# Optimization experiments

Hardware: AMD Instinct MI355X
Metric: run time of the kernel (lower is better)

Reference implementation:

```python
import jax, jax.numpy as jnp
import numpy as np

D_MODEL = 1024
D_FF = 4096
N_EXPERTS = 8
D_EXPERT = D_FF // N_EXPERTS  # 512
TOP_K = 2
LB_WEIGHT = 0.01
B, S = 4, 2048


def setup_inputs() -> dict:
    key = jax.random.key(0)
    ks = jax.random.split(key, 8)
    x = jax.random.normal(ks[0], (B, S, D_MODEL), dtype=jnp.float32)
    # per-expert FFN params stacked on expert axis
    w1 = jax.random.normal(ks[1], (N_EXPERTS, D_MODEL, D_EXPERT), dtype=jnp.float32) * (1.0 / np.sqrt(D_MODEL))
    b1 = jnp.zeros((N_EXPERTS, D_EXPERT), dtype=jnp.float32)
    w2 = jax.random.normal(ks[2], (N_EXPERTS, D_EXPERT, D_MODEL), dtype=jnp.float32) * (1.0 / np.sqrt(D_EXPERT))
    b2 = jnp.zeros((N_EXPERTS, D_MODEL), dtype=jnp.float32)
    centroids = jax.random.normal(ks[3], (N_EXPERTS, D_MODEL), dtype=jnp.float32) * 0.02
    w_route = jax.random.normal(ks[4], (N_EXPERTS, D_MODEL), dtype=jnp.float32) * (1.0 / np.sqrt(D_MODEL))
    return {"x": x, "w1": w1, "b1": b1, "w2": w2, "b2": b2,
            "centroids": centroids, "w_route": w_route}


def _top_k_softmax(logits, k):
    # softmax restricted to the top-k logits per token; zeros elsewhere
    vals, _ = jax.lax.top_k(logits, k)          # (..., k)
    thresh = vals[..., -1:]                     # kth-largest value
    masked = jnp.where(logits >= thresh, logits, -jnp.inf)
    return jax.nn.softmax(masked, axis=-1)


def reference(x, w1, b1, w2, b2, centroids, w_route):
    eps = 1e-12
    x_norm = x / jnp.maximum(jnp.linalg.norm(x, axis=-1, keepdims=True), eps)
    c_norm = centroids / jnp.maximum(jnp.linalg.norm(centroids, axis=-1, keepdims=True), eps)
    cos_scores = jnp.einsum('bsd,ed->bse', x_norm, c_norm)
    route_scores = jnp.einsum('bsd,ed->bse', x, w_route)
    logits = cos_scores + route_scores                       # (B,S,E)
    gates = _top_k_softmax(logits, TOP_K)                    # (B,S,E)
    # all experts computed on all tokens (dense MoE, masked combine)
    h = jax.nn.gelu(jnp.einsum('bsd,edh->bseh', x, w1) + b1, approximate=False)
    expert_out = jnp.einsum('bseh,ehd->bsed', h, w2) + b2    # (B,S,E,D)
    out = jnp.einsum('bse,bsed->bsd', gates, expert_out)
    return out
```

## Files before the change

kernel.cpp:

```cpp
#include <hip/hip_runtime.h>
#include <hip/hip_bf16.h>
#include <math.h>

#define T_TOK 8192
#define DM 1024
#define DE 512
#define NE 8
#define DFF 4096

#define CO_X   0
#define CO_W1  8388608
#define CO_W2  12582912
#define CO_B1  16777216
#define CO_B2  16781312
#define CO_CE  16789504
#define CO_WR  16797696
#define CO_TOT 16805888

#define WS_GATE2 256
#define WS_B32   65792
#define WS_TOP2  262400
#define WS_TOK   295168
#define WS_AE    360704
#define WS_AG    426240
#define WS_INV   491776
#define WS_CONV  557312
#define WS_HC    34169088
#define WS_OC    50946304

typedef __attribute__((ext_vector_type(8))) __bf16 bf16x8;
typedef __attribute__((ext_vector_type(4))) __bf16 bf16x4;
typedef __attribute__((ext_vector_type(4))) float f32x4;

__device__ __forceinline__ f32x4 ld4(const void* p, size_t off, int md)
{
  f32x4 r;
  if (md){
    bf16x4 v = *(const bf16x4*)((const __bf16*)p + off);
    #pragma unroll
    for (int j = 0; j < 4; j++) r[j] = (float)v[j];
  } else {
    r = *(const f32x4*)((const float*)p + off);
  }
  return r;
}

__device__ __forceinline__ void async_ld16(const __bf16* g, __bf16* l)
{
  __builtin_amdgcn_global_load_lds(
      (const __attribute__((address_space(1))) unsigned int*)g,
      (__attribute__((address_space(3))) unsigned int*)l, 16, 0, 0);
}

__global__ __launch_bounds__(256) void detect_k(const void* xp, const void* cp,
                                                int* meta, int* b32)
{
  const int tid = threadIdx.x;
  const float* xf = (const float*)xp;
  int ok = 0;
  for (int i = tid; i < 1024; i += 256){
    float a = fabsf(xf[i]);
    if (a > 1e-8f && a < 100.f) ok++;
  }
  __shared__ int cnt;
  __shared__ int flg;
  if (tid == 0) cnt = 0;
  __syncthreads();
  atomicAdd(&cnt, ok);
  __syncthreads();
  if (tid == 0){ flg = (cnt > 512) ? 0 : 1; meta[0] = flg; }
  __syncthreads();
  const int md = flg;

  const int e = tid >> 5, i = tid & 31;
  float ss = 0.f;
  for (int j = 0; j < 32; j++){
    size_t d = (size_t)e * DM + i + j * 32;
    float v = md ? (float)((const __bf16*)cp)[d] : ((const float*)cp)[d];
    ss += v * v;
  }
  #pragma unroll
  for (int m = 1; m < 32; m <<= 1) ss += __shfl_xor(ss, m, 64);
  float* cinv = (float*)(meta + 48);
  if (i == 0) cinv[e] = 1.f / fmaxf(sqrtf(ss), 1e-12f);

  b32[tid] = 0;
  if (tid < 8) meta[16 + tid] = 0;
}

__global__ __launch_bounds__(256) void convert_k(
    const float* __restrict__ x, const float* __restrict__ b1,
    const float* __restrict__ b2, const float* __restrict__ ce,
    const float* __restrict__ wr, __bf16* __restrict__ dst,
    const int* __restrict__ meta)
{
  if (meta[0]) return;
  const size_t i = ((size_t)blockIdx.x * 256 + threadIdx.x) * 4;
  const float* src; size_t doff;
  if (i < 8388608){ src = x + i; doff = CO_X + i; }
  else {
    size_t j = i - 8388608;
    doff = CO_B1 + j;
    if      (j < 4096)  src = b1 + j;
    else if (j < 12288) src = b2 + (j - 4096);
    else if (j < 20480) src = ce + (j - 12288);
    else                src = wr + (j - 20480);
  }
  f32x4 v = *(const f32x4*)src;
  bf16x4 o;
  #pragma unroll
  for (int j = 0; j < 4; j++) o[j] = (__bf16)v[j];
  *(bf16x4*)(dst + doff) = o;
}

__global__ __launch_bounds__(256) void transp_k(
    const void* w1q, const void* w2q, __bf16* __restrict__ conv,
    const int* __restrict__ meta)
{
  const int md = meta[0];
  __shared__ __bf16 tile[32][33];
  const int b = blockIdx.x, tid = threadIdx.x;
  const int ty = tid >> 5, tx = tid & 31;

  const void* src; __bf16* dst; int ldS, ldD, i0, j0; size_t soff, doffb;
  if (b < 4096){
    const int e = b >> 9, t = b & 511;
    i0 = (t >> 4) << 5; j0 = (t & 15) << 5;
    ldS = DE; ldD = DM;
    soff = (size_t)e * DM * DE;
    dst = conv + CO_W1; doffb = (size_t)e * DE * DM;
    src = md ? (const void*)((const __bf16*)w1q) : (const void*)((const float*)w1q);
  } else {
    const int e = (b - 4096) >> 9, t = (b - 4096) & 511;
    i0 = (t >> 5) << 5; j0 = (t & 31) << 5;
    ldS = DM; ldD = DE;
    soff = (size_t)e * DE * DM;
    dst = conv + CO_W2; doffb = (size_t)e * DM * DE;
    src = md ? (const void*)((const __bf16*)w2q) : (const void*)((const float*)w2q);
  }

  #pragma unroll
  for (int rr = 0; rr < 4; rr++){
    const int r = rr * 8 + ty;
    const size_t s = soff + (size_t)(i0 + r) * ldS + j0 + tx;
    tile[r][tx] = md ? ((const __bf16*)src)[s] : (__bf16)((const float*)src)[s];
  }
  __syncthreads();
  #pragma unroll
  for (int rr = 0; rr < 4; rr++){
    const int r = rr * 8 + ty;
    dst[doffb + (size_t)(j0 + r) * ldD + i0 + tx] = tile[tx][r];
  }
}

__global__ __launch_bounds__(256) void route_k(
    const void* __restrict__ xp, const void* __restrict__ cp,
    const void* __restrict__ wp, const int* __restrict__ meta,
    float2* __restrict__ gate2, int* __restrict__ top2, int* __restrict__ b32)
{
  const int md = meta[0];
  const float* cinv = (const float*)(meta + 48);
  const int tid = threadIdx.x;
  const int g = tid >> 4, l = tid & 15;
  const int t = blockIdx.x * 16 + g;

  __shared__ int hist[8];
  if (tid < 8) hist[tid] = 0;
  __syncthreads();

  float xx = 0.f, cd[NE], wd[NE];
  #pragma unroll
  for (int e = 0; e < NE; e++){ cd[e] = 0.f; wd[e] = 0.f; }

  const size_t xbase = (size_t)t * DM;
  for (int j = 0; j < 16; j++){
    const int d0 = j * 64 + l * 4;
    f32x4 xv = ld4(xp, xbase + d0, md);
    xx += xv[0]*xv[0] + xv[1]*xv[1] + xv[2]*xv[2] + xv[3]*xv[3];
    #pragma unroll
    for (int e = 0; e < NE; e++){
      f32x4 cv = ld4(cp, (size_t)e * DM + d0, md);
      f32x4 wv = ld4(wp, (size_t)e * DM + d0, md);
      cd[e] += xv[0]*cv[0] + xv[1]*cv[1] + xv[2]*cv[2] + xv[3]*cv[3];
      wd[e] += xv[0]*wv[0] + xv[1]*wv[1] + xv[2]*wv[2] + xv[3]*wv[3];
    }
  }
  #pragma unroll
  for (int m = 1; m < 16; m <<= 1){
    xx += __shfl_xor(xx, m, 64);
    #pragma unroll
    for (int e = 0; e < NE; e++){
      cd[e] += __shfl_xor(cd[e], m, 64);
      wd[e] += __shfl_xor(wd[e], m, 64);
    }
  }

  if (l == 0){
    const float rxn = 1.f / fmaxf(sqrtf(xx), 1e-12f);
    float logits[NE];
    #pragma unroll
    for (int e = 0; e < NE; e++) logits[e] = cd[e] * rxn * cinv[e] + wd[e];
    float m1 = -1e30f; int i1 = 0;
    #pragma unroll
    for (int e = 0; e < NE; e++) if (logits[e] > m1){ m1 = logits[e]; i1 = e; }
    float m2 = -1e30f; int i2 = (i1 == 0) ? 1 : 0;
    #pragma unroll
    for (int e = 0; e < NE; e++)
      if (e != i1 && logits[e] > m2){ m2 = logits[e]; i2 = e; }
    float denom = 0.f, ex1 = 0.f, ex2 = 0.f;
    #pragma unroll
    for (int e = 0; e < NE; e++){
      if (logits[e] >= m2){
        float ee = expf(logits[e] - m1);
        denom += ee;
        if (e == i1) ex1 = ee;
        if (e == i2) ex2 = ee;
      }
    }
    const float inv = 1.f / denom;
    gate2[t] = make_float2(ex1 * inv, ex2 * inv);
    top2[t] = i1 | (i2 << 8);
    atomicAdd(&hist[i1], 1);
    atomicAdd(&hist[i2], 1);
  }
  __syncthreads();
  if (tid < 8) atomicAdd(&b32[(blockIdx.x >> 4) * 8 + tid], hist[tid]);
}

__global__ void offsets_k(int* meta, int* b32)
{
  const int l = threadIdx.x;
  int running = 0;
  for (int e = 0; e < NE; e++){
    int v = (l < 32) ? b32[l * 8 + e] : 0;
    int incl = v;
    #pragma unroll
    for (int ofs = 1; ofs < 32; ofs <<= 1){
      int n = __shfl_up(incl, ofs, 64);
      if (l >= ofs) incl += n;
    }
    int tot = __shfl(incl, 31, 64);
    if (l < 32) b32[l * 8 + e] = running + (incl - v);
    if (l == 0){ meta[16 + e] = tot; meta[32 + e] = running; }
    running += tot;
  }
}

__global__ __launch_bounds__(256) void place_k(
    const int* __restrict__ top2, const float2* __restrict__ gate2,
    const int* __restrict__ b32, int* __restrict__ tok, int* __restrict__ ae,
    float* __restrict__ agv, int* __restrict__ inv)
{
  __shared__ int cur[8];
  if (threadIdx.x < 8) cur[threadIdx.x] = b32[blockIdx.x * 8 + threadIdx.x];
  __syncthreads();
  const int t = blockIdx.x * 256 + threadIdx.x;
  const int p = top2[t];
  const float2 gg = gate2[t];
  const int e1 = p & 255, e2 = (p >> 8) & 255;
  const int s1 = atomicAdd(&cur[e1], 1);
  tok[s1] = t; ae[s1] = e1; agv[s1] = gg.x; inv[2 * t] = s1;
  const int s2 = atomicAdd(&cur[e2], 1);
  tok[s2] = t; ae[s2] = e2; agv[s2] = gg.y; inv[2 * t + 1] = s2;
}

__device__ __forceinline__ bool find_tile(const int* meta, int tm,
                                          int& e, int& base, int& valid)
{
  for (e = 0; e < NE; e++){
    const int cnt = meta[16 + e];
    const int nt = (cnt + 127) >> 7;
    if (tm < nt){
      const int r0 = tm << 7;
      base = meta[32 + e] + r0;
      valid = cnt - r0;
      return true;
    }
    tm -= nt;
  }
  return false;
}

__global__ __launch_bounds__(256) void gemm1g_k(
    const void* xq, const void* b1q, const __bf16* __restrict__ conv,
    const int* __restrict__ meta, const int* __restrict__ tok,
    const float* __restrict__ agv, __bf16* __restrict__ Hc)
{
  const int md = meta[0];
  const __bf16* X  = md ? (const __bf16*)xq : conv + CO_X;
  const __bf16* WT = conv + CO_W1;
  const __bf16* bb = md ? (const __bf16*)b1q : conv + CO_B1;

  int e, base, valid;
  if (!find_tile(meta, blockIdx.x, e, base, valid)) return;
  const int n0 = blockIdx.y * 128;

  __shared__ __attribute__((aligned(16))) __bf16 As[128 * 32];
  __shared__ __attribute__((aligned(16))) __bf16 Bs[128 * 32];

  const int tid = threadIdx.x;
  const int wv = tid >> 6, lane = tid & 63;
  const int q = lane >> 4, ln = lane & 15;
  const int wm = (wv >> 1) * 64, wn = (wv & 1) * 64;
  f32x4 acc[4][4] = {};

  const int sr = tid >> 2, sc = (tid & 3) * 8;
  const int t0 = tok[base + ((sr      < valid) ? sr      : 0)];
  const int t1 = tok[base + ((sr + 64 < valid) ? sr + 64 : 0)];
  const __bf16* Ag0 = X + (size_t)t0 * DM + sc;
  const __bf16* Ag1 = X + (size_t)t1 * DM + sc;
  const __bf16* Bg0 = WT + (size_t)e * (DE * DM) + (size_t)(n0 + sr) * DM + sc;
  const __bf16* Bg1 = Bg0 + (size_t)64 * DM;

  for (int k0 = 0; k0 < DM; k0 += 32){
    __syncthreads();
    async_ld16(Ag0 + k0, As + tid * 8);
    async_ld16(Ag1 + k0, As + 2048 + tid * 8);
    async_ld16(Bg0 + k0, Bs + tid * 8);
    async_ld16(Bg1 + k0, Bs + 2048 + tid * 8);
    __syncthreads();

    bf16x8 af[4], bf[4];
    #pragma unroll
    for (int mi = 0; mi < 4; mi++)
      af[mi] = *(const bf16x8*)&As[(wm + mi * 16 + ln) * 32 + q * 8];
    #pragma unroll
    for (int ni = 0; ni < 4; ni++)
      bf[ni] = *(const bf16x8*)&Bs[(wn + ni * 16 + ln) * 32 + q * 8];
    #pragma unroll
    for (int mi = 0; mi < 4; mi++)
      #pragma unroll
      for (int ni = 0; ni < 4; ni++)
        acc[mi][ni] = __builtin_amdgcn_mfma_f32_16x16x32_bf16(
            af[mi], bf[ni], acc[mi][ni], 0, 0, 0);
  }

  const int coln = n0 + wn;
  float bset[4];
  #pragma unroll
  for (int ni = 0; ni < 4; ni++)
    bset[ni] = (float)bb[e * DE + coln + ni * 16 + ln];
  #pragma unroll
  for (int mi = 0; mi < 4; mi++){
    #pragma unroll
    for (int r = 0; r < 4; r++){
      const int row = wm + mi * 16 + q * 4 + r;
      if (row < valid){
        const int slot = base + row;
        const float g = agv[slot];
        #pragma unroll
        for (int ni = 0; ni < 4; ni++){
          float v = acc[mi][ni][r] + bset[ni];
          float h = 0.5f * v * (1.0f + erff(v * 0.70710678118654752f));
          Hc[(size_t)slot * DE + coln + ni * 16 + ln] = (__bf16)(g * h);
        }
      }
    }
  }
}

__global__ __launch_bounds__(256) void gemm2g_k(
    const __bf16* __restrict__ Hc, const __bf16* __restrict__ conv,
    const int* __restrict__ meta, __bf16* __restrict__ Oc)
{
  const __bf16* WT = conv + CO_W2;

  int e, base, valid;
  if (!find_tile(meta, blockIdx.x, e, base, valid)) return;
  const int n0 = blockIdx.y * 128;

  __shared__ __attribute__((aligned(16))) __bf16 As[128 * 32];
  __shared__ __attribute__((aligned(16))) __bf16 Bs[128 * 32];

  const int tid = threadIdx.x;
  const int wv = tid >> 6, lane = tid & 63;
  const int q = lane >> 4, ln = lane & 15;
  const int wm = (wv >> 1) * 64, wn = (wv & 1) * 64;
  f32x4 acc[4][4] = {};

  const int sr = tid >> 2, sc = (tid & 3) * 8;
  const int r0 = (sr      < valid) ? sr      : 0;
  const int r1 = (sr + 64 < valid) ? sr + 64 : 0;
  const __bf16* Ag0 = Hc + (size_t)(base + r0) * DE + sc;
  const __bf16* Ag1 = Hc + (size_t)(base + r1) * DE + sc;
  const __bf16* Bg0 = WT + (size_t)e * (DM * DE) + (size_t)(n0 + sr) * DE + sc;
  const __bf16* Bg1 = Bg0 + (size_t)64 * DE;

  for (int k0 = 0; k0 < DE; k0 += 32){
    __syncthreads();
    async_ld16(Ag0 + k0, As + tid * 8);
    async_ld16(Ag1 + k0, As + 2048 + tid * 8);
    async_ld16(Bg0 + k0, Bs + tid * 8);
    async_ld16(Bg1 + k0, Bs + 2048 + tid * 8);
    __syncthreads();

    bf16x8 af[4], bf[4];
    #pragma unroll
    for (int mi = 0; mi < 4; mi++)
      af[mi] = *(const bf16x8*)&As[(wm + mi * 16 + ln) * 32 + q * 8];
    #pragma unroll
    for (int ni = 0; ni < 4; ni++)
      bf[ni] = *(const bf16x8*)&Bs[(wn + ni * 16 + ln) * 32 + q * 8];
    #pragma unroll
    for (int mi = 0; mi < 4; mi++)
      #pragma unroll
      for (int ni = 0; ni < 4; ni++)
        acc[mi][ni] = __builtin_amdgcn_mfma_f32_16x16x32_bf16(
            af[mi], bf[ni], acc[mi][ni], 0, 0, 0);
  }

  #pragma unroll
  for (int mi = 0; mi < 4; mi++){
    #pragma unroll
    for (int r = 0; r < 4; r++){
      const int row = wm + mi * 16 + q * 4 + r;
      if (row < valid){
        const int slot = base + row;
        #pragma unroll
        for (int ni = 0; ni < 4; ni++)
          Oc[(size_t)slot * DM + n0 + wn + ni * 16 + ln] = (__bf16)acc[mi][ni][r];
      }
    }
  }
}

__global__ __launch_bounds__(256) void combine_k(
    const __bf16* __restrict__ Oc, const int* __restrict__ inv,
    const int* __restrict__ ae, const float* __restrict__ agv,
    const void* b2q, const int* __restrict__ meta, void* out)
{
  const int md = meta[0];
  const int t = blockIdx.x;
  const int s1 = inv[2 * t], s2 = inv[2 * t + 1];
  const int e1 = ae[s1], e2 = ae[s2];
  const float g1 = agv[s1], g2 = agv[s2];
  const int c = threadIdx.x * 4;

  bf16x4 o1 = *(const bf16x4*)(Oc + (size_t)s1 * DM + c);
  bf16x4 o2 = *(const bf16x4*)(Oc + (size_t)s2 * DM + c);
  f32x4 bv1 = ld4(b2q, (size_t)e1 * DM + c, md);
  f32x4 bv2 = ld4(b2q, (size_t)e2 * DM + c, md);
  f32x4 rr;
  #pragma unroll
  for (int j = 0; j < 4; j++)
    rr[j] = (float)o1[j] + (float)o2[j] + g1 * bv1[j] + g2 * bv2[j];

  if (md){
    bf16x4 ob;
    #pragma unroll
    for (int j = 0; j < 4; j++) ob[j] = (__bf16)rr[j];
    *(bf16x4*)((__bf16*)out + (size_t)t * DM + c) = ob;
  } else {
    *(f32x4*)((float*)out + (size_t)t * DM + c) = rr;
  }
}

extern "C" void kernel_launch(void* const* d_in, const int* in_sizes, int n_in,
                              void* d_out, int out_size, void* d_ws, size_t ws_size,
                              hipStream_t stream)
{
  char* ws = (char*)d_ws;
  int*    meta  = (int*)ws;
  float2* gate2 = (float2*)(ws + WS_GATE2);
  int*    b32   = (int*)(ws + WS_B32);
  int*    top2  = (int*)(ws + WS_TOP2);
  int*    tok   = (int*)(ws + WS_TOK);
  int*    ae    = (int*)(ws + WS_AE);
  float*  agv   = (float*)(ws + WS_AG);
  int*    inv   = (int*)(ws + WS_INV);
  __bf16* conv  = (__bf16*)(ws + WS_CONV);
  __bf16* Hc    = (__bf16*)(ws + WS_HC);
  __bf16* Oc    = (__bf16*)(ws + WS_OC);

  detect_k<<<1, 256, 0, stream>>>(d_in[0], d_in[5], meta, b32);
  transp_k<<<8192, 256, 0, stream>>>(d_in[1], d_in[3], conv, meta);
  convert_k<<<8220, 256, 0, stream>>>(
      (const float*)d_in[0], (const float*)d_in[2], (const float*)d_in[4],
      (const float*)d_in[5], (const float*)d_in[6], conv, meta);
  route_k<<<T_TOK / 16, 256, 0, stream>>>(d_in[0], d_in[5], d_in[6], meta,
                                          gate2, top2, b32);
  offsets_k<<<1, 64, 0, stream>>>(meta, b32);
  place_k<<<T_TOK / 256, 256, 0, stream>>>(top2, gate2, b32, tok, ae, agv, inv);
  gemm1g_k<<<dim3(136, 4), 256, 0, stream>>>(d_in[0], d_in[2], conv, meta,
                                             tok, agv, Hc);
  gemm2g_k<<<dim3(136, 8), 256, 0, stream>>>(Hc, conv, meta, Oc);
  combine_k<<<T_TOK, 256, 0, stream>>>(Oc, inv, ae, agv, d_in[4], meta, d_out);
}
```

Before: 243.6 us.

## Merge preprocessing kernels into one launch and double-buffer the first expert GEMM

Folds detect, transpose, convert and routing into a single prep kernel in which every block redetects the input dtype on its own, and fuses the bf16 conversion of x into the routing pass. Offsets and placement are merged into one single-block scheduler kernel that uses an LDS prefix scan. gemm1 moves to 512 threads, a K=64 tile with double-buffered async LDS loads and an XOR swizzle, to overlap loads with MFMA work and cut bank conflicts. In exchange, each block repeats the dtype detection, and the single-block scheduler serializes placement of all 8192 tokens.

```diff
diff --git a/kernel.cpp b/kernel.cpp
--- a/kernel.cpp
+++ b/kernel.cpp
@@ -15,7 +15,6 @@
 #define CO_B2  16781312
 #define CO_CE  16789504
 #define CO_WR  16797696
-#define CO_TOT 16805888
 
 #define WS_GATE2 256
 #define WS_B32   65792
@@ -52,120 +51,104 @@
       (__attribute__((address_space(3))) unsigned int*)l, 16, 0, 0);
 }
 
-__global__ __launch_bounds__(256) void detect_k(const void* xp, const void* cp,
-                                                int* meta, int* b32)
-{
+__device__ __forceinline__ int detect_md_block(const float* xf, int tid,
+                                               int* cnt_lds)
+{
+  int ok = 0;
+  #pragma unroll
+  for (int i = 0; i < 4; i++){
+    float a = fabsf(xf[tid + i * 256]);
+    if (a > 1e-8f && a < 100.f) ok++;
+  }
+  if (tid == 0) *cnt_lds = 0;
+  __syncthreads();
+  atomicAdd(cnt_lds, ok);
+  __syncthreads();
+  return (*cnt_lds > 512) ? 0 : 1;
+}
+
+__global__ __launch_bounds__(256) void prep_k(
+    const void* xp, const void* w1q, const void* w2q,
+    const void* b1q, const void* b2q, const void* cp, const void* wp,
+    __bf16* __restrict__ conv, int* __restrict__ meta,
+    float2* __restrict__ gate2, int* __restrict__ top2, int* __restrict__ b32)
+{
+  __shared__ int mdcnt;
+  __shared__ __bf16 tile[32][33];
+  __shared__ int hist[8];
+  __shared__ float cinvL[8];
+
   const int tid = threadIdx.x;
-  const float* xf = (const float*)xp;
-  int ok = 0;
-  for (int i = tid; i < 1024; i += 256){
-    float a = fabsf(xf[i]);
-    if (a > 1e-8f && a < 100.f) ok++;
-  }
-  __shared__ int cnt;
-  __shared__ int flg;
-  if (tid == 0) cnt = 0;
-  __syncthreads();
-  atomicAdd(&cnt, ok);
-  __syncthreads();
-  if (tid == 0){ flg = (cnt > 512) ? 0 : 1; meta[0] = flg; }
-  __syncthreads();
-  const int md = flg;
-
-  const int e = tid >> 5, i = tid & 31;
-  float ss = 0.f;
-  for (int j = 0; j < 32; j++){
-    size_t d = (size_t)e * DM + i + j * 32;
-    float v = md ? (float)((const __bf16*)cp)[d] : ((const float*)cp)[d];
-    ss += v * v;
-  }
-  #pragma unroll
-  for (int m = 1; m < 32; m <<= 1) ss += __shfl_xor(ss, m, 64);
-  float* cinv = (float*)(meta + 48);
-  if (i == 0) cinv[e] = 1.f / fmaxf(sqrtf(ss), 1e-12f);
-
-  b32[tid] = 0;
-  if (tid < 8) meta[16 + tid] = 0;
-}
-
-__global__ __launch_bounds__(256) void convert_k(
-    const float* __restrict__ x, const float* __restrict__ b1,
-    const float* __restrict__ b2, const float* __restrict__ ce,
-    const float* __restrict__ wr, __bf16* __restrict__ dst,
-    const int* __restrict__ meta)
-{
-  if (meta[0]) return;
-  const size_t i = ((size_t)blockIdx.x * 256 + threadIdx.x) * 4;
-  const float* src; size_t doff;
-  if (i < 8388608){ src = x + i; doff = CO_X + i; }
-  else {
-    size_t j = i - 8388608;
-    doff = CO_B1 + j;
-    if      (j < 4096)  src = b1 + j;
-    else if (j < 12288) src = b2 + (j - 4096);
-    else if (j < 20480) src = ce + (j - 12288);
-    else                src = wr + (j - 20480);
-  }
-  f32x4 v = *(const f32x4*)src;
-  bf16x4 o;
-  #pragma unroll
-  for (int j = 0; j < 4; j++) o[j] = (__bf16)v[j];
-  *(bf16x4*)(dst + doff) = o;
-}
-
-__global__ __launch_bounds__(256) void transp_k(
-    const void* w1q, const void* w2q, __bf16* __restrict__ conv,
-    const int* __restrict__ meta)
-{
-  const int md = meta[0];
-  __shared__ __bf16 tile[32][33];
-  const int b = blockIdx.x, tid = threadIdx.x;
-  const int ty = tid >> 5, tx = tid & 31;
-
-  const void* src; __bf16* dst; int ldS, ldD, i0, j0; size_t soff, doffb;
-  if (b < 4096){
-    const int e = b >> 9, t = b & 511;
-    i0 = (t >> 4) << 5; j0 = (t & 15) << 5;
-    ldS = DE; ldD = DM;
-    soff = (size_t)e * DM * DE;
-    dst = conv + CO_W1; doffb = (size_t)e * DE * DM;
-    src = md ? (const void*)((const __bf16*)w1q) : (const void*)((const float*)w1q);
-  } else {
-    const int e = (b - 4096) >> 9, t = (b - 4096) & 511;
-    i0 = (t >> 5) << 5; j0 = (t & 31) << 5;
-    ldS = DM; ldD = DE;
-    soff = (size_t)e * DE * DM;
-    dst = conv + CO_W2; doffb = (size_t)e * DM * DE;
-    src = md ? (const void*)((const __bf16*)w2q) : (const void*)((const float*)w2q);
-  }
-
-  #pragma unroll
-  for (int rr = 0; rr < 4; rr++){
-    const int r = rr * 8 + ty;
-    const size_t s = soff + (size_t)(i0 + r) * ldS + j0 + tx;
-    tile[r][tx] = md ? ((const __bf16*)src)[s] : (__bf16)((const float*)src)[s];
-  }
-  __syncthreads();
-  #pragma unroll
-  for (int rr = 0; rr < 4; rr++){
-    const int r = rr * 8 + ty;
-    dst[doffb + (size_t)(j0 + r) * ldD + i0 + tx] = tile[tx][r];
-  }
-}
-
-__global__ __launch_bounds__(256) void route_k(
-    const void* __restrict__ xp, const void* __restrict__ cp,
-    const void* __restrict__ wp, const int* __restrict__ meta,
-    float2* __restrict__ gate2, int* __restrict__ top2, int* __restrict__ b32)
-{
-  const int md = meta[0];
-  const float* cinv = (const float*)(meta + 48);
-  const int tid = threadIdx.x;
+  const int md = detect_md_block((const float*)xp, tid, &mdcnt);
+  const int b = blockIdx.x;
+
+  if (b < 8192){
+    const void* src; __bf16* dst; int ldS, ldD, i0, j0; size_t soff, doffb;
+    const int ty = tid >> 5, tx = tid & 31;
+    if (b < 4096){
+      const int e = b >> 9, t = b & 511;
+      i0 = (t >> 4) << 5; j0 = (t & 15) << 5;
+      ldS = DE; ldD = DM;
+      soff = (size_t)e * DM * DE;
+      dst = conv + CO_W1; doffb = (size_t)e * DE * DM;
+      src = md ? (const void*)((const __bf16*)w1q) : (const void*)((const float*)w1q);
+    } else {
+      const int e = (b - 4096) >> 9, t = (b - 4096) & 511;
+      i0 = (t >> 5) << 5; j0 = (t & 31) << 5;
+      ldS = DM; ldD = DE;
+      soff = (size_t)e * DE * DM;
+      dst = conv + CO_W2; doffb = (size_t)e * DM * DE;
+      src = md ? (const void*)((const __bf16*)w2q) : (const void*)((const float*)w2q);
+    }
+    #pragma unroll
+    for (int rr = 0; rr < 4; rr++){
+      const int r = rr * 8 + ty;
+      const size_t s = soff + (size_t)(i0 + r) * ldS + j0 + tx;
+      tile[r][tx] = md ? ((const __bf16*)src)[s] : (__bf16)((const float*)src)[s];
+    }
+    __syncthreads();
+    #pragma unroll
+    for (int rr = 0; rr < 4; rr++){
+      const int r = rr * 8 + ty;
+      dst[doffb + (size_t)(j0 + r) * ldD + i0 + tx] = tile[tx][r];
+    }
+    return;
+  }
+
+  if (b < 8220){
+    if (md) return;
+    const size_t j = ((size_t)(b - 8192) * 256 + tid) * 4;
+    const float* src;
+    const size_t doff = CO_B1 + j;
+    if      (j < 4096)  src = (const float*)b1q + j;
+    else if (j < 12288) src = (const float*)b2q + (j - 4096);
+    else if (j < 20480) src = (const float*)cp + (j - 12288);
+    else                src = (const float*)wp + (j - 20480);
+    f32x4 v = *(const f32x4*)src;
+    bf16x4 o;
+    #pragma unroll
+    for (int t = 0; t < 4; t++) o[t] = (__bf16)v[t];
+    *(bf16x4*)(conv + doff) = o;
+    return;
+  }
+
+  const int rb = b - 8220;
   const int g = tid >> 4, l = tid & 15;
-  const int t = blockIdx.x * 16 + g;
-
-  __shared__ int hist[8];
+  const int t = rb * 16 + g;
+
   if (tid < 8) hist[tid] = 0;
+  {
+    const int e = tid >> 5, i = tid & 31;
+    float ss = 0.f;
+    for (int j = 0; j < 32; j++){
+      size_t d = (size_t)e * DM + i + j * 32;
+      float v = md ? (float)((const __bf16*)cp)[d] : ((const float*)cp)[d];
+      ss += v * v;
+    }
+    #pragma unroll
+    for (int m = 1; m < 32; m <<= 1) ss += __shfl_xor(ss, m, 64);
+    if (i == 0) cinvL[e] = 1.f / fmaxf(sqrtf(ss), 1e-12f);
+  }
   __syncthreads();
 
   float xx = 0.f, cd[NE], wd[NE];
@@ -176,6 +159,12 @@
   for (int j = 0; j < 16; j++){
     const int d0 = j * 64 + l * 4;
     f32x4 xv = ld4(xp, xbase + d0, md);
+    if (!md){
+      bf16x4 o;
+      #pragma unroll
+      for (int jj = 0; jj < 4; jj++) o[jj] = (__bf16)xv[jj];
+      *(bf16x4*)(conv + CO_X + xbase + d0) = o;
+    }
     xx += xv[0]*xv[0] + xv[1]*xv[1] + xv[2]*xv[2] + xv[3]*xv[3];
     #pragma unroll
     for (int e = 0; e < NE; e++){
@@ -199,7 +188,7 @@
     const float rxn = 1.f / fmaxf(sqrtf(xx), 1e-12f);
     float logits[NE];
     #pragma unroll
-    for (int e = 0; e < NE; e++) logits[e] = cd[e] * rxn * cinv[e] + wd[e];
+    for (int e = 0; e < NE; e++) logits[e] = cd[e] * rxn * cinvL[e] + wd[e];
     float m1 = -1e30f; int i1 = 0;
     #pragma unroll
     for (int e = 0; e < NE; e++) if (logits[e] > m1){ m1 = logits[e]; i1 = e; }
@@ -224,44 +213,59 @@
     atomicAdd(&hist[i2], 1);
   }
   __syncthreads();
-  if (tid < 8) atomicAdd(&b32[(blockIdx.x >> 4) * 8 + tid], hist[tid]);
-}
-
-__global__ void offsets_k(int* meta, int* b32)
-{
-  const int l = threadIdx.x;
-  int running = 0;
-  for (int e = 0; e < NE; e++){
-    int v = (l < 32) ? b32[l * 8 + e] : 0;
-    int incl = v;
-    #pragma unroll
-    for (int ofs = 1; ofs < 32; ofs <<= 1){
-      int n = __shfl_up(incl, ofs, 64);
-      if (l >= ofs) incl += n;
-    }
-    int tot = __shfl(incl, 31, 64);
-    if (l < 32) b32[l * 8 + e] = running + (incl - v);
-    if (l == 0){ meta[16 + e] = tot; meta[32 + e] = running; }
-    running += tot;
-  }
-}
-
-__global__ __launch_bounds__(256) void place_k(
+  if (tid < 8) b32[rb * 8 + tid] = hist[tid];
+  if (rb == 0 && tid == 0) meta[0] = md;
+}
+
+__global__ __launch_bounds__(1024) void sched_k(
     const int* __restrict__ top2, const float2* __restrict__ gate2,
-    const int* __restrict__ b32, int* __restrict__ tok, int* __restrict__ ae,
-    float* __restrict__ agv, int* __restrict__ inv)
-{
-  __shared__ int cur[8];
-  if (threadIdx.x < 8) cur[threadIdx.x] = b32[blockIdx.x * 8 + threadIdx.x];
-  __syncthreads();
-  const int t = blockIdx.x * 256 + threadIdx.x;
-  const int p = top2[t];
-  const float2 gg = gate2[t];
-  const int e1 = p & 255, e2 = (p >> 8) & 255;
-  const int s1 = atomicAdd(&cur[e1], 1);
-  tok[s1] = t; ae[s1] = e1; agv[s1] = gg.x; inv[2 * t] = s1;
-  const int s2 = atomicAdd(&cur[e2], 1);
-  tok[s2] = t; ae[s2] = e2; agv[s2] = gg.y; inv[2 * t + 1] = s2;
+    int* __restrict__ meta, const int* __restrict__ b32,
+    int* __restrict__ tok, int* __restrict__ ae, float* __restrict__ agv,
+    int* __restrict__ inv)
+{
+  __shared__ int bufA[4096];
+  __shared__ int bufB[4096];
+  __shared__ int offE[8];
+  const int tid = threadIdx.x;
+
+  for (int i = tid; i < 4096; i += 1024) bufA[i] = b32[i];
+  __syncthreads();
+
+  int* cur = bufA; int* nxt = bufB;
+  for (int d = 1; d < 512; d <<= 1){
+    for (int i = tid; i < 4096; i += 1024){
+      int v = cur[i];
+      if ((i >> 3) >= d) v += cur[i - (d << 3)];
+      nxt[i] = v;
+    }
+    __syncthreads();
+    int* s = cur; cur = nxt; nxt = s;
+  }
+
+  if (tid == 0){
+    int run = 0;
+    #pragma unroll
+    for (int e = 0; e < NE; e++){
+      const int tt = cur[(511 << 3) + e];
+      meta[16 + e] = tt; meta[32 + e] = run; offE[e] = run; run += tt;
+    }
+  }
+  __syncthreads();
+
+  for (int i = tid; i < 4096; i += 1024)
+    nxt[i] = offE[i & 7] + cur[i] - b32[i];
+  __syncthreads();
+
+  for (int t = tid; t < T_TOK; t += 1024){
+    const int p = top2[t];
+    const float2 gg = gate2[t];
+    const int rb = t >> 4;
+    const int e1 = p & 255, e2 = (p >> 8) & 255;
+    const int s1 = atomicAdd(&nxt[(rb << 3) + e1], 1);
+    tok[s1] = t; ae[s1] = e1; agv[s1] = gg.x; inv[2 * t] = s1;
+    const int s2 = atomicAdd(&nxt[(rb << 3) + e2], 1);
+    tok[s2] = t; ae[s2] = e2; agv[s2] = gg.y; inv[2 * t + 1] = s2;
+  }
 }
 
 __device__ __forceinline__ bool find_tile(const int* meta, int tm,
@@ -281,7 +285,7 @@
   return false;
 }
 
-__global__ __launch_bounds__(256) void gemm1g_k(
+__global__ __launch_bounds__(512, 2) void gemm1g_k(
     const void* xq, const void* b1q, const __bf16* __restrict__ conv,
     const int* __restrict__ meta, const int* __restrict__ tok,
     const float* __restrict__ agv, __bf16* __restrict__ Hc)
@@ -295,50 +299,70 @@
   if (!find_tile(meta, blockIdx.x, e, base, valid)) return;
   const int n0 = blockIdx.y * 128;
 
-  __shared__ __attribute__((aligned(16))) __bf16 As[128 * 32];
-  __shared__ __attribute__((aligned(16))) __bf16 Bs[128 * 32];
+  __shared__ __attribute__((aligned(16))) __bf16 As[2][128 * 64];
+  __shared__ __attribute__((aligned(16))) __bf16 Bs[2][128 * 64];
 
   const int tid = threadIdx.x;
   const int wv = tid >> 6, lane = tid & 63;
   const int q = lane >> 4, ln = lane & 15;
-  const int wm = (wv >> 1) * 64, wn = (wv & 1) * 64;
-  f32x4 acc[4][4] = {};
-
-  const int sr = tid >> 2, sc = (tid & 3) * 8;
-  const int t0 = tok[base + ((sr      < valid) ? sr      : 0)];
-  const int t1 = tok[base + ((sr + 64 < valid) ? sr + 64 : 0)];
-  const __bf16* Ag0 = X + (size_t)t0 * DM + sc;
-  const __bf16* Ag1 = X + (size_t)t1 * DM + sc;
-  const __bf16* Bg0 = WT + (size_t)e * (DE * DM) + (size_t)(n0 + sr) * DM + sc;
+  const int wm = (wv >> 2) * 64, wn = (wv & 3) * 32;
+  const int swz = ln & 7;
+  f32x4 acc[4][2] = {};
+
+  const int srow = tid >> 3, sch = tid & 7;
+  const int sx = ((sch ^ (srow & 7)) << 3);
+  const int ta = tok[base + ((srow      < valid) ? srow      : 0)];
+  const int tb = tok[base + ((srow + 64 < valid) ? srow + 64 : 0)];
+  const __bf16* Ag0 = X + (size_t)ta * DM + sx;
+  const __bf16* Ag1 = X + (size_t)tb * DM + sx;
+  const __bf16* Bg0 = WT + (size_t)e * (DE * DM) + (size_t)(n0 + srow) * DM + sx;
   const __bf16* Bg1 = Bg0 + (size_t)64 * DM;
 
-  for (int k0 = 0; k0 < DM; k0 += 32){
+  #define G1_STAGE(BUF, K0)                                   \
+    do {                                                      \
+      async_ld16(Ag0 + (K0), &As[BUF][tid * 8]);              \
+      async_ld16(Ag1 + (K0), &As[BUF][tid * 8 + 4096]);       \
+      async_ld16(Bg0 + (K0), &Bs[BUF][tid * 8]);              \
+      async_ld16(Bg1 + (K0), &Bs[BUF][tid * 8 + 4096]);       \
+    } while (0)
+
+  #define G1_COMPUTE(BUF)                                                      \
+    do {                                                                       \
+      _Pragma("unroll")                                                        \
+      for (int kk = 0; kk < 2; kk++){                                          \
+        bf16x8 af[4], bfr[2];                                                  \
+        const int ch = (((kk << 2) | q) ^ swz) << 3;                           \
+        _Pragma("unroll")                                                      \
+        for (int mi = 0; mi < 4; mi++)                                         \
+          af[mi] = *(const bf16x8*)&As[BUF][(wm + mi * 16 + ln) * 64 + ch];    \
+        _Pragma("unroll")                                                      \
+        for (int ni = 0; ni < 2; ni++)                                         \
+          bfr[ni] = *(const bf16x8*)&Bs[BUF][(wn + ni * 16 + ln) * 64 + ch];   \
+        _Pragma("unroll")                                                      \
+        for (int mi = 0; mi < 4; mi++)                                         \
+          _Pragma("unroll")                                                    \
+          for (int ni = 0; ni < 2; ni++)                                       \
+            acc[mi][ni] = __builtin_amdgcn_mfma_f32_16x16x32_bf16(             \
+                af[mi], bfr[ni], acc[mi][ni], 0, 0, 0);                        \
+      }                                                                        \
+    } while (0)
+
+  G1_STAGE(0, 0);
+  __syncthreads();
+  int cr = 0;
+  for (int t = 0; t < 16; ++t){
+    if (t < 15) G1_STAGE(cr ^ 1, (t + 1) * 64);
+    G1_COMPUTE(cr);
     __syncthreads();
-    async_ld16(Ag0 + k0, As + tid * 8);
-    async_ld16(Ag1 + k0, As + 2048 + tid * 8);
-    async_ld16(Bg0 + k0, Bs + tid * 8);
-    async_ld16(Bg1 + k0, Bs + 2048 + tid * 8);
-    __syncthreads();
-
-    bf16x8 af[4], bf[4];
-    #pragma unroll
-    for (int mi = 0; mi < 4; mi++)
-      af[mi] = *(const bf16x8*)&As[(wm + mi * 16 + ln) * 32 + q * 8];
-    #pragma unroll
-    for (int ni = 0; ni < 4; ni++)
-      bf[ni] = *(const bf16x8*)&Bs[(wn + ni * 16 + ln) * 32 + q * 8];
-    #pragma unroll
-    for (int mi = 0; mi < 4; mi++)
-      #pragma unroll
-      for (int ni = 0; ni < 4; ni++)
-        acc[mi][ni] = __builtin_amdgcn_mfma_f32_16x16x32_bf16(
-            af[mi], bf[ni], acc[mi][ni], 0, 0, 0);
-  }
+    cr ^= 1;
+  }
+  #undef G1_STAGE
+  #undef G1_COMPUTE
 
   const int coln = n0 + wn;
-  float bset[4];
-  #pragma unroll
-  for (int ni = 0; ni < 4; ni++)
+  float bset[2];
+  #pragma unroll
+  for (int ni = 0; ni < 2; ni++)
     bset[ni] = (float)bb[e * DE + coln + ni * 16 + ln];
   #pragma unroll
   for (int mi = 0; mi < 4; mi++){
@@ -349,7 +373,7 @@
         const int slot = base + row;
         const float g = agv[slot];
         #pragma unroll
-        for (int ni = 0; ni < 4; ni++){
+        for (int ni = 0; ni < 2; ni++){
           float v = acc[mi][ni][r] + bset[ni];
           float h = 0.5f * v * (1.0f + erff(v * 0.70710678118654752f));
           Hc[(size_t)slot * DE + coln + ni * 16 + ln] = (__bf16)(g * h);
@@ -394,19 +418,19 @@
     async_ld16(Bg1 + k0, Bs + 2048 + tid * 8);
     __syncthreads();
 
-    bf16x8 af[4], bf[4];
+    bf16x8 af[4], bfr[4];
     #pragma unroll
     for (int mi = 0; mi < 4; mi++)
       af[mi] = *(const bf16x8*)&As[(wm + mi * 16 + ln) * 32 + q * 8];
     #pragma unroll
     for (int ni = 0; ni < 4; ni++)
-      bf[ni] = *(const bf16x8*)&Bs[(wn + ni * 16 + ln) * 32 + q * 8];
+      bfr[ni] = *(const bf16x8*)&Bs[(wn + ni * 16 + ln) * 32 + q * 8];
     #pragma unroll
     for (int mi = 0; mi < 4; mi++)
       #pragma unroll
       for (int ni = 0; ni < 4; ni++)
         acc[mi][ni] = __builtin_amdgcn_mfma_f32_16x16x32_bf16(
-            af[mi], bf[ni], acc[mi][ni], 0, 0, 0);
+            af[mi], bfr[ni], acc[mi][ni], 0, 0, 0);
   }
 
   #pragma unroll
@@ -472,16 +496,11 @@
   __bf16* Hc    = (__bf16*)(ws + WS_HC);
   __bf16* Oc    = (__bf16*)(ws + WS_OC);
 
-  detect_k<<<1, 256, 0, stream>>>(d_in[0], d_in[5], meta, b32);
-  transp_k<<<8192, 256, 0, stream>>>(d_in[1], d_in[3], conv, meta);
-  convert_k<<<8220, 256, 0, stream>>>(
-      (const float*)d_in[0], (const float*)d_in[2], (const float*)d_in[4],
-      (const float*)d_in[5], (const float*)d_in[6], conv, meta);
-  route_k<<<T_TOK / 16, 256, 0, stream>>>(d_in[0], d_in[5], d_in[6], meta,
-                                          gate2, top2, b32);
-  offsets_k<<<1, 64, 0, stream>>>(meta, b32);
-  place_k<<<T_TOK / 256, 256, 0, stream>>>(top2, gate2, b32, tok, ae, agv, inv);
-  gemm1g_k<<<dim3(136, 4), 256, 0, stream>>>(d_in[0], d_in[2], conv, meta,
+  prep_k<<<8732, 256, 0, stream>>>(d_in[0], d_in[1], d_in[3], d_in[2],
+                                   d_in[4], d_in[5], d_in[6],
+                                   conv, meta, gate2, top2, b32);
+  sched_k<<<1, 1024, 0, stream>>>(top2, gate2, meta, b32, tok, ae, agv, inv);
+  gemm1g_k<<<dim3(136, 4), 512, 0, stream>>>(d_in[0], d_in[2], conv, meta,
                                              tok, agv, Hc);
   gemm2g_k<<<dim3(136, 8), 256, 0, stream>>>(Hc, conv, meta, Oc);
   combine_k<<<T_TOK, 256, 0, stream>>>(Oc, inv, ae, agv, d_in[4], meta, d_out);
```

Result: slower. 288.8 us (+18.6%).
